# Kernel tuning notes

Hardware: AMD Instinct MI355X
Metric: run time of the kernel (lower is better)

Reference implementation:

```python
import jax, jax.numpy as jnp
import numpy as np

B, F, N = 8, 64, 256
EPS = 1e-09


def setup_inputs() -> dict:
    key = jax.random.key(0)
    k = jax.random.split(key, 4)
    x = jax.random.normal(k[0], (B, F, N, N), dtype=jnp.float32)
    mask = jax.random.randint(k[1], (B, N), 0, 2).astype(jnp.float32)
    weight = jnp.ones((1, F, 1, 1), dtype=jnp.float32)
    weight_exp = jax.random.normal(k[2], (1, F, 1, 1), dtype=jnp.float32)
    weight_bias = jnp.zeros((1, F, 1, 1), dtype=jnp.float32)
    bias = jax.random.normal(k[3], (1, F, 1), dtype=jnp.float32)
    return dict(x=x, mask=mask, weight=weight, weight_exp=weight_exp,
                weight_bias=weight_bias, bias=bias)


def reference(x, mask, weight, weight_exp, weight_bias, bias):
    # mask: [B, N] -> pairwise mask [B, 1, N, N] (broadcast over features,
    # same math as torch .expand to [B, F, N, N])
    m2 = mask[:, None, :, None] * mask[:, None, None, :]
    mdiag = mask * mask                       # diagonal of pairwise mask, [B, N]
    n = jnp.sum(mdiag, axis=-1, keepdims=True)  # [B, 1] (identical across F)
    n2 = jnp.clip(n - 1.0, 1.0)

    # trace(A * mask) per (b, f)
    diagA = jnp.einsum('bfii->bfi', x)
    trace = jnp.sum(diagA * mdiag[:, None, :], axis=-1)        # [B, F]
    # trace(A^2 * mask): diag(A @ A)_i = sum_k A[i,k] A[k,i]  (O(N^2), same math
    # as torch.linalg.matrix_power(A, 2) followed by masked diagonal trace)
    diagA2 = jnp.einsum('bfik,bfki->bfi', x, x)
    trace_sq = jnp.sum(diagA2 * mdiag[:, None, :], axis=-1)    # [B, F]

    mean = trace / n
    variance = trace_sq / n2 - trace ** 2 / (n * n2)
    mean_b = mean.mean(axis=1)      # [B]
    var_b = variance.mean(axis=1)   # [B]

    eye = jnp.eye(N, dtype=x.dtype)
    m_t = mean_b[:, None, None, None] * eye          # diag_embed of mean
    x_centered = (x - m_t) * m2
    x_norm = x_centered / jnp.sqrt(var_b[:, None, None, None] + EPS)

    bias_diag = bias[..., None] * eye                # [1, F, N, N] diag_embed
    return x_norm * (weight * jnp.exp(weight_exp) + weight_bias) + bias_diag
```

## Files before the change

kernel.cpp:

```cpp
#include <hip/hip_runtime.h>
#include <math.h>

#define BB 8
#define FF 64
#define NN 256
#define EPSF 1e-9f

typedef float floatx4 __attribute__((ext_vector_type(4)));


__device__ __forceinline__ int fit(int e) {
    constexpr int IT[10] = {0,1,2,3, 0,0,0,1,1,2};
    return IT[e];
}
__device__ __forceinline__ int fkt(int e) {
    constexpr int KT[10] = {0,1,2,3, 1,2,3,2,3,3};
    return KT[e];
}

__global__ __launch_bounds__(256, 6) void k_traces(const float* __restrict__ x,
                                                   const float* __restrict__ mask,
                                                   float* __restrict__ ws) {
    __shared__ float T1[64][65];
    __shared__ float mdi[64], mdk[64];
    __shared__ float red[4][2];

    const int t   = threadIdx.x;
    const int mat = blockIdx.x;
    const int job = blockIdx.y;
    const int b   = mat >> 6;
    const int i0  = fit(job) << 6;
    const int k0  = fkt(job) << 6;
    const bool diag = (job < 4);
    const float* __restrict__ xm = x + (size_t)mat * (NN * NN);

    if (t < 64)       { float m = mask[b * NN + i0 + t];      mdi[t]      = m * m; }
    else if (t < 128) { float m = mask[b * NN + k0 + t - 64]; mdk[t - 64] = m * m; }

    const int la  = t >> 4;
    const int lc4 = (t & 15) << 2;
    const int lane = t & 63;
    const int w    = t >> 6;

    float4 p[4];
    float4 u[4];
    #pragma unroll
    for (int rr = 0; rr < 4; ++rr) {
        const int a = la + (rr << 4);
        p[rr] = *(const float4*)(xm + (size_t)(i0 + a) * NN + k0 + lc4);
        if (!diag)
            u[rr] = *(const float4*)(xm + (size_t)(k0 + a) * NN + i0 + lc4);
    }
    #pragma unroll
    for (int rr = 0; rr < 4; ++rr) {
        const int a = la + (rr << 4);
        T1[a][lc4 + 0] = p[rr].x; T1[a][lc4 + 1] = p[rr].y;
        T1[a][lc4 + 2] = p[rr].z; T1[a][lc4 + 3] = p[rr].w;
    }
    __syncthreads();

    float acc2 = 0.f, trp = 0.f;
    if (!diag) {
        #pragma unroll
        for (int rr = 0; rr < 4; ++rr) {
            const int c = la + (rr << 4);
            const float mk = mdk[c];
            acc2 += T1[lc4 + 0][c] * u[rr].x * (mdi[lc4 + 0] + mk);
            acc2 += T1[lc4 + 1][c] * u[rr].y * (mdi[lc4 + 1] + mk);
            acc2 += T1[lc4 + 2][c] * u[rr].z * (mdi[lc4 + 2] + mk);
            acc2 += T1[lc4 + 3][c] * u[rr].w * (mdi[lc4 + 3] + mk);
        }
    } else {
        #pragma unroll
        for (int s = 0; s < 16; ++s) {
            const int a = w + (s << 2);
            acc2 += T1[a][lane] * T1[lane][a] * mdi[a];
            if (lane == a) trp += T1[a][a] * mdi[a];
        }
    }

    #pragma unroll
    for (int off = 32; off > 0; off >>= 1) {
        acc2 += __shfl_down(acc2, off);
        trp  += __shfl_down(trp,  off);
    }
    if (lane == 0) { red[w][0] = trp; red[w][1] = acc2; }
    __syncthreads();
    if (t == 0) {
        ws[(mat << 4) + job]        = red[0][0] + red[1][0] + red[2][0] + red[3][0];
        ws[8192 + (mat << 4) + job] = red[0][1] + red[1][1] + red[2][1] + red[3][1];
    }
}

__global__ __launch_bounds__(256) void k_out(const float* __restrict__ x,
                                             const float* __restrict__ mask,
                                             const float* __restrict__ wt,
                                             const float* __restrict__ wexp,
                                             const float* __restrict__ wbias,
                                             const float* __restrict__ bias,
                                             const float* __restrict__ ws,
                                             float* __restrict__ out) {
    __shared__ float md[NN];
    __shared__ float sstats[4];

    const int t   = threadIdx.x;
    const int mat = blockIdx.x;
    const int q   = blockIdx.y;
    const int b   = mat >> 6;
    const int f   = mat & 63;

    { float m = mask[(b << 8) + t]; md[t] = m * m; }

    const int lane = t & 63;
    const int w    = t >> 6;

    if (w == 0) {
        const int base = ((b << 6) + lane) << 4;
        float trf = 0.f, tsf = 0.f;
        #pragma unroll
        for (int j = 0; j < 10; ++j) {
            trf += ws[base + j];
            tsf += ws[8192 + base + j];
        }
        float tr2 = trf * trf;
        float m0 = mask[(b << 8) + lane];
        float m1 = mask[(b << 8) + lane + 64];
        float m2 = mask[(b << 8) + lane + 128];
        float m3 = mask[(b << 8) + lane + 192];
        float nn = m0 * m0 + m1 * m1 + m2 * m2 + m3 * m3;
        #pragma unroll
        for (int off = 32; off > 0; off >>= 1) {
            trf += __shfl_down(trf, off);
            tr2 += __shfl_down(tr2, off);
            tsf += __shfl_down(tsf, off);
            nn  += __shfl_down(nn,  off);
        }
        if (lane == 0) {
            float n  = nn;
            float n2 = fmaxf(n - 1.f, 1.f);
            sstats[0] = trf / (64.f * n);
            sstats[1] = 1.f / sqrtf(tsf / (64.f * n2) - tr2 / (64.f * n * n2) + EPSF);
            sstats[2] = wt[f] * expf(wexp[f]) + wbias[f];
            sstats[3] = bias[f];
        }
    }
    __syncthreads();

    const float meanb = sstats[0];
    const float istd  = sstats[1];
    const float gs    = sstats[2];
    const float bs    = sstats[3];
    const float* __restrict__ xm = x + (size_t)mat * (NN * NN);
    float* __restrict__       om = out + (size_t)mat * (NN * NN);

    const int r0 = q << 6;
    const int j0 = lane << 2;
    const float4 mj = *(const float4*)&md[j0];
    const float mjx = mj.x * istd * gs, mjy = mj.y * istd * gs,
                mjz = mj.z * istd * gs, mjw = mj.w * istd * gs;

    #pragma unroll
    for (int rr = 0; rr < 16; ++rr) {
        const int i = r0 + w + (rr << 2);
        const float4 xv = *(const float4*)(xm + (size_t)i * NN + j0);
        const float mi = md[i];
        floatx4 o;
        o.x = (xv.x - (i == j0     ? meanb : 0.f)) * mjx * mi + (i == j0     ? bs : 0.f);
        o.y = (xv.y - (i == j0 + 1 ? meanb : 0.f)) * mjy * mi + (i == j0 + 1 ? bs : 0.f);
        o.z = (xv.z - (i == j0 + 2 ? meanb : 0.f)) * mjz * mi + (i == j0 + 2 ? bs : 0.f);
        o.w = (xv.w - (i == j0 + 3 ? meanb : 0.f)) * mjw * mi + (i == j0 + 3 ? bs : 0.f);
        *(floatx4*)(om + (size_t)i * NN + j0) = o;
    }
}

extern "C" void kernel_launch(void* const* d_in, const int* in_sizes, int n_in,
                              void* d_out, int out_size, void* d_ws, size_t ws_size,
                              hipStream_t stream) {
    const float* x     = (const float*)d_in[0];
    const float* mask  = (const float*)d_in[1];
    const float* wt    = (const float*)d_in[2];
    const float* wexp  = (const float*)d_in[3];
    const float* wbias = (const float*)d_in[4];
    const float* bias  = (const float*)d_in[5];
    float* out = (float*)d_out;
    float* ws  = (float*)d_ws;

    hipLaunchKernelGGL(k_traces, dim3(512, 10), dim3(256), 0, stream, x, mask, ws);
    hipLaunchKernelGGL(k_out,    dim3(512, 4),  dim3(256), 0, stream,
                       x, mask, wt, wexp, wbias, bias, ws, out);
}
```

Baseline: 63.65 us.

## Fuse trace and output kernels into one cooperative persistent kernel with grid sync

Replaces the two-kernel sequence with a single cooperative persistent kernel. Each block first computes trace partials for half-matrix work units, then does a grid-wide sync, then writes normalized output for the same units, so the second x read may still hit L2/MALL. Output stores are now nontemporal. The host queries occupancy and device attributes on every launch, and the grid sync plus lower occupancy could cost more than the kernel boundary it removes.

```diff
diff --git a/kernel.cpp b/kernel.cpp
--- a/kernel.cpp
+++ b/kernel.cpp
@@ -1,5 +1,8 @@
 #include <hip/hip_runtime.h>
+#include <hip/hip_cooperative_groups.h>
 #include <math.h>
+
+namespace cg = cooperative_groups;
 
 #define BB 8
 #define FF 64
@@ -7,6 +10,168 @@
 #define EPSF 1e-9f
 
 typedef float floatx4 __attribute__((ext_vector_type(4)));
+
+
+__device__ __forceinline__ int jit(int half, int e) {
+    constexpr int IT0[5] = {0, 1, 0, 0, 0};
+    constexpr int IT1[5] = {2, 3, 1, 1, 2};
+    return half ? IT1[e] : IT0[e];
+}
+__device__ __forceinline__ int jkt(int half, int e) {
+    constexpr int KT0[5] = {0, 1, 1, 2, 3};
+    constexpr int KT1[5] = {2, 3, 2, 3, 3};
+    return half ? KT1[e] : KT0[e];
+}
+
+__global__ __launch_bounds__(256, 4) void k_fused(
+    const float* __restrict__ x, const float* __restrict__ mask,
+    const float* __restrict__ wt, const float* __restrict__ wexp,
+    const float* __restrict__ wbias, const float* __restrict__ bias,
+    float* __restrict__ out, float* __restrict__ ws) {
+
+    __shared__ float md[NN];
+    __shared__ float T1[64][65];
+    __shared__ float red[4][2];
+    __shared__ float sstats[4];
+
+    const int t    = threadIdx.x;
+    const int G    = gridDim.x;
+    const int lane = t & 63;
+    const int w    = t >> 6;
+    const int la   = t >> 4;
+    const int lc4  = (t & 15) << 2;
+
+    for (int v = blockIdx.x; v < 1024; v += G) {
+        const int mat  = v >> 1;
+        const int half = v & 1;
+        const int b    = mat >> 6;
+        const float* __restrict__ xm = x + (size_t)mat * (NN * NN);
+
+        __syncthreads();
+        { float m = mask[(b << 8) + t]; md[t] = m * m; }
+
+        float acc2 = 0.f, trp = 0.f;
+        #pragma unroll
+        for (int e = 0; e < 5; ++e) {
+            const bool diag = (e < 2);
+            const int i0 = jit(half, e) << 6;
+            const int k0 = jkt(half, e) << 6;
+            float4 p[4], u[4];
+            #pragma unroll
+            for (int rr = 0; rr < 4; ++rr) {
+                const int a = la + (rr << 4);
+                p[rr] = *(const float4*)(xm + (size_t)(i0 + a) * NN + k0 + lc4);
+                if (!diag)
+                    u[rr] = *(const float4*)(xm + (size_t)(k0 + a) * NN + i0 + lc4);
+            }
+            __syncthreads();
+            #pragma unroll
+            for (int rr = 0; rr < 4; ++rr) {
+                const int a = la + (rr << 4);
+                T1[a][lc4 + 0] = p[rr].x; T1[a][lc4 + 1] = p[rr].y;
+                T1[a][lc4 + 2] = p[rr].z; T1[a][lc4 + 3] = p[rr].w;
+            }
+            __syncthreads();
+            if (!diag) {
+                #pragma unroll
+                for (int rr = 0; rr < 4; ++rr) {
+                    const int c = la + (rr << 4);
+                    const float mk = md[k0 + c];
+                    acc2 += T1[lc4 + 0][c] * u[rr].x * (md[i0 + lc4 + 0] + mk);
+                    acc2 += T1[lc4 + 1][c] * u[rr].y * (md[i0 + lc4 + 1] + mk);
+                    acc2 += T1[lc4 + 2][c] * u[rr].z * (md[i0 + lc4 + 2] + mk);
+                    acc2 += T1[lc4 + 3][c] * u[rr].w * (md[i0 + lc4 + 3] + mk);
+                }
+            } else {
+                #pragma unroll
+                for (int s = 0; s < 16; ++s) {
+                    const int a = w + (s << 2);
+                    acc2 += T1[a][lane] * T1[lane][a] * md[i0 + a];
+                    if (lane == a) trp += T1[a][a] * md[i0 + a];
+                }
+            }
+        }
+
+        #pragma unroll
+        for (int off = 32; off > 0; off >>= 1) {
+            acc2 += __shfl_down(acc2, off);
+            trp  += __shfl_down(trp,  off);
+        }
+        if (lane == 0) { red[w][0] = trp; red[w][1] = acc2; }
+        __syncthreads();
+        if (t == 0) {
+            float trace = red[0][0] + red[1][0] + red[2][0] + red[3][0];
+            float tsq   = red[0][1] + red[1][1] + red[2][1] + red[3][1];
+            __hip_atomic_store(&ws[v],        trace, __ATOMIC_RELAXED, __HIP_MEMORY_SCOPE_AGENT);
+            __hip_atomic_store(&ws[1024 + v], tsq,   __ATOMIC_RELAXED, __HIP_MEMORY_SCOPE_AGENT);
+        }
+    }
+
+    cg::this_grid().sync();
+
+    for (int v = blockIdx.x; v < 1024; v += G) {
+        const int mat  = v >> 1;
+        const int half = v & 1;
+        const int b    = mat >> 6;
+        const int f    = mat & 63;
+
+        __syncthreads();
+        { float m = mask[(b << 8) + t]; md[t] = m * m; }
+        __syncthreads();
+
+        if (w == 0) {
+            const int base = (b << 7) + (lane << 1);
+            float trf = __hip_atomic_load(&ws[base],            __ATOMIC_RELAXED, __HIP_MEMORY_SCOPE_AGENT)
+                      + __hip_atomic_load(&ws[base + 1],        __ATOMIC_RELAXED, __HIP_MEMORY_SCOPE_AGENT);
+            float tsf = __hip_atomic_load(&ws[1024 + base],     __ATOMIC_RELAXED, __HIP_MEMORY_SCOPE_AGENT)
+                      + __hip_atomic_load(&ws[1024 + base + 1], __ATOMIC_RELAXED, __HIP_MEMORY_SCOPE_AGENT);
+            float tr2 = trf * trf;
+            float nn  = md[lane] + md[lane + 64] + md[lane + 128] + md[lane + 192];
+            #pragma unroll
+            for (int off = 32; off > 0; off >>= 1) {
+                trf += __shfl_down(trf, off);
+                tr2 += __shfl_down(tr2, off);
+                tsf += __shfl_down(tsf, off);
+                nn  += __shfl_down(nn,  off);
+            }
+            if (lane == 0) {
+                float n  = nn;
+                float n2 = fmaxf(n - 1.f, 1.f);
+                sstats[0] = trf / (64.f * n);
+                sstats[1] = 1.f / sqrtf(tsf / (64.f * n2) - tr2 / (64.f * n * n2) + EPSF);
+                sstats[2] = wt[f] * expf(wexp[f]) + wbias[f];
+                sstats[3] = bias[f];
+            }
+        }
+        __syncthreads();
+
+        const float meanb = sstats[0];
+        const float istd  = sstats[1];
+        const float gs    = sstats[2];
+        const float bs    = sstats[3];
+        const float* __restrict__ xm = x + (size_t)mat * (NN * NN);
+        float* __restrict__       om = out + (size_t)mat * (NN * NN);
+
+        const int r0 = half << 7;
+        const int j0 = lane << 2;
+        const float4 mj = *(const float4*)&md[j0];
+        const float mjx = mj.x * istd * gs, mjy = mj.y * istd * gs,
+                    mjz = mj.z * istd * gs, mjw = mj.w * istd * gs;
+
+        #pragma unroll
+        for (int rr = 0; rr < 32; ++rr) {
+            const int i = r0 + w + (rr << 2);
+            const float4 xv = *(const float4*)(xm + (size_t)i * NN + j0);
+            const float mi = md[i];
+            floatx4 o;
+            o.x = (xv.x - (i == j0     ? meanb : 0.f)) * mjx * mi + (i == j0     ? bs : 0.f);
+            o.y = (xv.y - (i == j0 + 1 ? meanb : 0.f)) * mjy * mi + (i == j0 + 1 ? bs : 0.f);
+            o.z = (xv.z - (i == j0 + 2 ? meanb : 0.f)) * mjz * mi + (i == j0 + 2 ? bs : 0.f);
+            o.w = (xv.w - (i == j0 + 3 ? meanb : 0.f)) * mjw * mi + (i == j0 + 3 ? bs : 0.f);
+            __builtin_nontemporal_store(o, (floatx4*)(om + (size_t)i * NN + j0));
+        }
+    }
+}
 
 
 __device__ __forceinline__ int fit(int e) {
@@ -42,8 +207,7 @@
     const int lane = t & 63;
     const int w    = t >> 6;
 
-    float4 p[4];
-    float4 u[4];
+    float4 p[4], u[4];
     #pragma unroll
     for (int rr = 0; rr < 4; ++rr) {
         const int a = la + (rr << 4);
@@ -185,6 +349,25 @@
     float* out = (float*)d_out;
     float* ws  = (float*)d_ws;
 
+    int dev = 0;
+    (void)hipGetDevice(&dev);
+    int nCU = 0;
+    (void)hipDeviceGetAttribute(&nCU, hipDeviceAttributeMultiprocessorCount, dev);
+    int maxb = 0;
+    (void)hipOccupancyMaxActiveBlocksPerMultiprocessor(&maxb, (const void*)k_fused, 256, 0);
+
+    if (maxb > 0 && nCU > 0) {
+        long cap = (long)maxb * (long)nCU;
+        int G = (int)(cap < 1024 ? cap : 1024);
+        void* args[] = {(void*)&x, (void*)&mask, (void*)&wt, (void*)&wexp,
+                        (void*)&wbias, (void*)&bias, (void*)&out, (void*)&ws};
+        if (hipLaunchCooperativeKernel((const void*)k_fused, dim3(G), dim3(256),
+                                       args, 0, stream) == hipSuccess) {
+            return;
+        }
+        (void)hipGetLastError();
+    }
+
     hipLaunchKernelGGL(k_traces, dim3(512, 10), dim3(256), 0, stream, x, mask, ws);
     hipLaunchKernelGGL(k_out,    dim3(512, 4),  dim3(256), 0, stream,
                        x, mask, wt, wexp, wbias, bias, ws, out);
```

Result: slower. 133.4 us (+109.5%).
